# Kernel tuning notes

Measured on AMD Instinct MI355X. Metric: run time of the kernel, lower is better.

The kernel has to match this reference:

```python
import jax, jax.numpy as jnp
import numpy as np

N = 80
NUM_ITER = 100
TOL = 0.01


def _power_iteration_batched(A):
    # A: [B, d, d] batch of predecessor-probability matrices.
    # Faithful batched version of the original sequential power_iteration with
    # per-matrix early stopping emulated via a 'done' mask (converged entries
    # are frozen at the v_new computed on their break step, like the original).
    B, d, _ = A.shape
    v0 = jnp.ones((B, d), A.dtype) / jnp.sqrt(jnp.asarray(d, A.dtype))
    Av0 = jnp.einsum('bij,bj->bi', A, v0)
    ev0 = jnp.einsum('bi,bi->b', v0, Av0)
    done0 = jnp.zeros((B,), dtype=bool)

    def step(carry, _):
        v, ev, done = carry
        Av = jnp.einsum('bij,bj->bi', A, v)
        v_new = Av / jnp.linalg.norm(Av, axis=-1, keepdims=True)
        ev_new = jnp.einsum('bi,bij,bj->b', v_new, A, v_new)
        conv = jnp.abs(ev - ev_new) < TOL
        v_next = jnp.where(done[:, None], v, v_new)
        ev_next = jnp.where(done, ev, ev_new)
        return (v_next, ev_next, done | conv), None

    (v, ev, _), _ = jax.lax.scan(step, (v0, ev0, done0), None, length=NUM_ITER)
    return ev, v


def setup_inputs() -> dict:
    key = jax.random.key(0)
    k1, k2, k3, k4, k5 = jax.random.split(key, 5)
    return {
        'x': jax.random.uniform(k1, (N, N), dtype=jnp.float32),
        'r_zeros': jax.random.uniform(k2, (N, N, N, N), dtype=jnp.float32),
        'r_const': jax.random.uniform(k3, (N, N, N, N), dtype=jnp.float32),
        'weights_t': jax.random.uniform(k4, (N, N), dtype=jnp.float32),
        'weights_r': jax.random.uniform(k5, (N, N, N, N), dtype=jnp.float32),
    }


def reference(x, r_zeros, r_const, weights_t, weights_r):
    n = x.shape[0]
    ar = jnp.arange(n)
    # T_val[s,t] = layer2[s,t,s,s] = (x*weights_t)[s,t] * r_const[s,t,s,s]
    r_const_diag = r_const[ar[:, None], ar[None, :], ar[:, None], ar[:, None]]  # [N,N]
    T_val = (x * weights_t) * r_const_diag
    # weights_r_comb[s,t] = weights_r[s,t]*r_zeros[s,t] + r_const[s,t]
    M = (weights_r * r_zeros + r_const).reshape(n * n, n, n)
    _, v = _power_iteration_batched(M)          # v: [N*N, N]
    v = v.reshape(n, n, n)                      # [s, t, node]
    denom = v[ar[:, None], ar[None, :], ar[:, None]]  # v[s,t,s] -> [N,N]
    contrib = (v / denom[..., None]) * T_val[..., None]  # [N,N,N]
    return jnp.sum(contrib, axis=(0, 1))        # rbc_arr: [N]
```

## Files before the change

### kernel.cpp

```cpp
#include <hip/hip_runtime.h>

#define NDIM 80
#define NB (NDIM * NDIM)
#define MAT_ELEMS (NDIM * NDIM)
#define LDM 81
#define NUM_ITER 100
#define TOL 0.01f

__global__ __launch_bounds__(320) void power_iter_kernel(
    const float* __restrict__ r_zeros,
    const float* __restrict__ r_const,
    const float* __restrict__ weights_r,
    float* __restrict__ V)
{
    __shared__ float M[NDIM * LDM];
    __shared__ float v[NDIM];
    __shared__ float av[NDIM];
    __shared__ float red;

    const int t = threadIdx.x;
    const size_t base = (size_t)blockIdx.x * MAT_ELEMS;
    const float4* rz4 = reinterpret_cast<const float4*>(r_zeros + base);
    const float4* rc4 = reinterpret_cast<const float4*>(r_const + base);
    const float4* wr4 = reinterpret_cast<const float4*>(weights_r + base);

    for (int f = t; f < MAT_ELEMS / 4; f += 320) {
        float4 a = rz4[f];
        float4 c = rc4[f];
        float4 w = wr4[f];
        int e = f * 4;
        int i = e / NDIM;
        int j = e - i * NDIM;
        float* dst = &M[i * LDM + j];
        dst[0] = fmaf(w.x, a.x, c.x);
        dst[1] = fmaf(w.y, a.y, c.y);
        dst[2] = fmaf(w.z, a.z, c.z);
        dst[3] = fmaf(w.w, a.w, c.w);
    }
    if (t < NDIM) v[t] = 0.11180339887498949f;
    __syncthreads();

    const int r = t >> 2;
    const int q = t & 3;

    auto matvec = [&]() {
        float p = 0.f;
        const float* Mr = &M[r * LDM + q * 20];
        const float* vq = &v[q * 20];
        #pragma unroll
        for (int k = 0; k < 20; ++k) p = fmaf(Mr[k], vq[k], p);
        p += __shfl_xor(p, 1);
        p += __shfl_xor(p, 2);
        if (q == 0) av[r] = p;
        __syncthreads();
    };

    auto reduce_dot = [&]() {
        if (t < 64) {
            float s = v[t] * av[t];
            if (t < 16) s += v[t + 64] * av[t + 64];
            #pragma unroll
            for (int o = 32; o > 0; o >>= 1) s += __shfl_down(s, o);
            if (t == 0) red = s;
        }
        __syncthreads();
    };

    matvec();
    reduce_dot();
    float ev = red;

    for (int it = 0; it < NUM_ITER; ++it) {
        __syncthreads();
        if (t < 64) {
            float s = av[t] * av[t];
            if (t < 16) s += av[t + 64] * av[t + 64];
            #pragma unroll
            for (int o = 32; o > 0; o >>= 1) s += __shfl_down(s, o);
            if (t == 0) red = sqrtf(s);
        }
        __syncthreads();
        float nrm = red;
        if (t < NDIM) v[t] = av[t] / nrm;
        __syncthreads();
        matvec();
        reduce_dot();
        float evn = red;
        if (fabsf(ev - evn) < TOL) break;
        ev = evn;
    }

    if (t < NDIM) V[(size_t)blockIdx.x * NDIM + t] = v[t];
}

__global__ void scale_kernel(const float* __restrict__ x,
                             const float* __restrict__ r_const,
                             const float* __restrict__ wt,
                             const float* __restrict__ V,
                             float* __restrict__ scale)
{
    int b = blockIdx.x * blockDim.x + threadIdx.x;
    if (b >= NB) return;
    int i = b / NDIM;
    float tval = x[b] * wt[b] * r_const[((size_t)b * NDIM + i) * NDIM + i];
    scale[b] = tval / V[(size_t)b * NDIM + i];
}

__global__ __launch_bounds__(256) void out_kernel(
    const float* __restrict__ V,
    const float* __restrict__ scale,
    float* __restrict__ out)
{
    __shared__ float s[256];
    const int k = blockIdx.x;
    const int t = threadIdx.x;
    float acc = 0.f;
    for (int b = t; b < NB; b += 256)
        acc = fmaf(V[(size_t)b * NDIM + k], scale[b], acc);
    s[t] = acc;
    __syncthreads();
    for (int o = 128; o > 0; o >>= 1) {
        if (t < o) s[t] += s[t + o];
        __syncthreads();
    }
    if (t == 0) out[k] = s[0];
}

extern "C" void kernel_launch(void* const* d_in, const int* in_sizes, int n_in,
                              void* d_out, int out_size, void* d_ws, size_t ws_size,
                              hipStream_t stream) {
    const float* x  = (const float*)d_in[0];
    const float* rz = (const float*)d_in[1];
    const float* rc = (const float*)d_in[2];
    const float* wt = (const float*)d_in[3];
    const float* wr = (const float*)d_in[4];
    float* out = (float*)d_out;

    float* V     = (float*)d_ws;
    float* scale = V + (size_t)NB * NDIM;

    hipLaunchKernelGGL(power_iter_kernel, dim3(NB), dim3(320), 0, stream,
                       rz, rc, wr, V);
    hipLaunchKernelGGL(scale_kernel, dim3((NB + 255) / 256), dim3(256), 0, stream,
                       x, rc, wt, V, scale);
    hipLaunchKernelGGL(out_kernel, dim3(NDIM), dim3(256), 0, stream,
                       V, scale, out);
}
```

Baseline: 105.4 us.

## Fuse power iteration with output reduction, keep matrix rows in registers

Each thread now holds its 20 matrix elements in registers instead of staging the whole matrix in shared memory. The norm and the Rayleigh-quotient dot product are computed in one combined reduction pass, which drops a barrier phase per iteration. The scale and output kernels are folded into the power kernel through per-block atomicAdd into a zeroed output, removing the V and scale round trips and two launches. In exchange it adds atomic contention on 80 outputs, leaves summation order nondeterministic, and raises register pressure under a launch bound of 6 blocks.

Measured after the change: 176.1 us. 67.1% more time.

```diff
diff --git a/kernel.cpp b/kernel.cpp
--- a/kernel.cpp
+++ b/kernel.cpp
@@ -2,128 +2,98 @@
 
 #define NDIM 80
 #define NB (NDIM * NDIM)
-#define MAT_ELEMS (NDIM * NDIM)
-#define LDM 81
-#define NUM_ITER 100
 #define TOL 0.01f
+#define MAXIT 101
 
-__global__ __launch_bounds__(320) void power_iter_kernel(
+__global__ void zero_out_kernel(float* __restrict__ out) {
+    if (threadIdx.x < NDIM) out[threadIdx.x] = 0.f;
+}
+
+__global__ __launch_bounds__(320, 6) void fused_power_kernel(
+    const float* __restrict__ x,
     const float* __restrict__ r_zeros,
     const float* __restrict__ r_const,
+    const float* __restrict__ weights_t,
     const float* __restrict__ weights_r,
-    float* __restrict__ V)
+    float* __restrict__ out)
 {
-    __shared__ float M[NDIM * LDM];
     __shared__ float v[NDIM];
     __shared__ float av[NDIM];
-    __shared__ float red;
+    __shared__ float red[2];
+    __shared__ float sscale;
 
     const int t = threadIdx.x;
-    const size_t base = (size_t)blockIdx.x * MAT_ELEMS;
-    const float4* rz4 = reinterpret_cast<const float4*>(r_zeros + base);
-    const float4* rc4 = reinterpret_cast<const float4*>(r_const + base);
-    const float4* wr4 = reinterpret_cast<const float4*>(weights_r + base);
+    const int b = blockIdx.x;
+    const size_t base = (size_t)b * NB;
+    const int r = t >> 2;
+    const int q = t & 3;
+    const size_t off = base + (size_t)r * NDIM + q * 20;
 
-    for (int f = t; f < MAT_ELEMS / 4; f += 320) {
-        float4 a = rz4[f];
-        float4 c = rc4[f];
-        float4 w = wr4[f];
-        int e = f * 4;
-        int i = e / NDIM;
-        int j = e - i * NDIM;
-        float* dst = &M[i * LDM + j];
-        dst[0] = fmaf(w.x, a.x, c.x);
-        dst[1] = fmaf(w.y, a.y, c.y);
-        dst[2] = fmaf(w.z, a.z, c.z);
-        dst[3] = fmaf(w.w, a.w, c.w);
+    float m[20];
+    {
+        const float4* a4 = reinterpret_cast<const float4*>(r_zeros + off);
+        const float4* c4 = reinterpret_cast<const float4*>(r_const + off);
+        const float4* w4 = reinterpret_cast<const float4*>(weights_r + off);
+        #pragma unroll
+        for (int u = 0; u < 5; ++u) {
+            float4 a = a4[u], c = c4[u], w = w4[u];
+            m[4*u+0] = fmaf(w.x, a.x, c.x);
+            m[4*u+1] = fmaf(w.y, a.y, c.y);
+            m[4*u+2] = fmaf(w.z, a.z, c.z);
+            m[4*u+3] = fmaf(w.w, a.w, c.w);
+        }
     }
-    if (t < NDIM) v[t] = 0.11180339887498949f;
+
+    if (t < NDIM) av[t] = 1.0f;
+    float n2 = (float)NDIM;
+    float ev = 1e30f;
     __syncthreads();
 
-    const int r = t >> 2;
-    const int q = t & 3;
+    for (int it = 0; it < MAXIT; ++it) {
+        float inv = rsqrtf(n2);
+        if (t < NDIM) v[t] = av[t] * inv;
+        __syncthreads();
 
-    auto matvec = [&]() {
         float p = 0.f;
-        const float* Mr = &M[r * LDM + q * 20];
-        const float* vq = &v[q * 20];
+        const int vq = q * 20;
         #pragma unroll
-        for (int k = 0; k < 20; ++k) p = fmaf(Mr[k], vq[k], p);
+        for (int k = 0; k < 20; ++k) p = fmaf(m[k], v[vq + k], p);
         p += __shfl_xor(p, 1);
         p += __shfl_xor(p, 2);
         if (q == 0) av[r] = p;
         __syncthreads();
-    };
 
-    auto reduce_dot = [&]() {
         if (t < 64) {
-            float s = v[t] * av[t];
-            if (t < 16) s += v[t + 64] * av[t + 64];
+            float a0 = av[t], v0 = v[t];
+            float s2 = a0 * a0;
+            float sd = v0 * a0;
+            if (t < 16) {
+                float a1 = av[t + 64], v1 = v[t + 64];
+                s2 = fmaf(a1, a1, s2);
+                sd = fmaf(v1, a1, sd);
+            }
             #pragma unroll
-            for (int o = 32; o > 0; o >>= 1) s += __shfl_down(s, o);
-            if (t == 0) red = s;
+            for (int o = 32; o > 0; o >>= 1) {
+                s2 += __shfl_down(s2, o);
+                sd += __shfl_down(sd, o);
+            }
+            if (t == 0) { red[0] = s2; red[1] = sd; }
         }
         __syncthreads();
-    };
-
-    matvec();
-    reduce_dot();
-    float ev = red;
-
-    for (int it = 0; it < NUM_ITER; ++it) {
-        __syncthreads();
-        if (t < 64) {
-            float s = av[t] * av[t];
-            if (t < 16) s += av[t + 64] * av[t + 64];
-            #pragma unroll
-            for (int o = 32; o > 0; o >>= 1) s += __shfl_down(s, o);
-            if (t == 0) red = sqrtf(s);
-        }
-        __syncthreads();
-        float nrm = red;
-        if (t < NDIM) v[t] = av[t] / nrm;
-        __syncthreads();
-        matvec();
-        reduce_dot();
-        float evn = red;
+        n2 = red[0];
+        float evn = red[1];
         if (fabsf(ev - evn) < TOL) break;
         ev = evn;
     }
 
-    if (t < NDIM) V[(size_t)blockIdx.x * NDIM + t] = v[t];
-}
-
-__global__ void scale_kernel(const float* __restrict__ x,
-                             const float* __restrict__ r_const,
-                             const float* __restrict__ wt,
-                             const float* __restrict__ V,
-                             float* __restrict__ scale)
-{
-    int b = blockIdx.x * blockDim.x + threadIdx.x;
-    if (b >= NB) return;
-    int i = b / NDIM;
-    float tval = x[b] * wt[b] * r_const[((size_t)b * NDIM + i) * NDIM + i];
-    scale[b] = tval / V[(size_t)b * NDIM + i];
-}
-
-__global__ __launch_bounds__(256) void out_kernel(
-    const float* __restrict__ V,
-    const float* __restrict__ scale,
-    float* __restrict__ out)
-{
-    __shared__ float s[256];
-    const int k = blockIdx.x;
-    const int t = threadIdx.x;
-    float acc = 0.f;
-    for (int b = t; b < NB; b += 256)
-        acc = fmaf(V[(size_t)b * NDIM + k], scale[b], acc);
-    s[t] = acc;
+    if (t == 0) {
+        int i_idx = b / NDIM;
+        float tval = x[b] * weights_t[b]
+                   * r_const[base + (size_t)i_idx * NDIM + i_idx];
+        sscale = tval / v[i_idx];
+    }
     __syncthreads();
-    for (int o = 128; o > 0; o >>= 1) {
-        if (t < o) s[t] += s[t + o];
-        __syncthreads();
-    }
-    if (t == 0) out[k] = s[0];
+    if (t < NDIM) atomicAdd(&out[t], v[t] * sscale);
 }
 
 extern "C" void kernel_launch(void* const* d_in, const int* in_sizes, int n_in,
@@ -136,13 +106,7 @@
     const float* wr = (const float*)d_in[4];
     float* out = (float*)d_out;
 
-    float* V     = (float*)d_ws;
-    float* scale = V + (size_t)NB * NDIM;
-
-    hipLaunchKernelGGL(power_iter_kernel, dim3(NB), dim3(320), 0, stream,
-                       rz, rc, wr, V);
-    hipLaunchKernelGGL(scale_kernel, dim3((NB + 255) / 256), dim3(256), 0, stream,
-                       x, rc, wt, V, scale);
-    hipLaunchKernelGGL(out_kernel, dim3(NDIM), dim3(256), 0, stream,
-                       V, scale, out);
+    hipLaunchKernelGGL(zero_out_kernel, dim3(1), dim3(128), 0, stream, out);
+    hipLaunchKernelGGL(fused_power_kernel, dim3(NB), dim3(320), 0, stream,
+                       x, rz, rc, wt, wr, out);
 }
```
